# Performance work log

Measured on AMD Instinct MI355X. Metric: run time of the kernel, lower is better.

## Reference

```python
import jax, jax.numpy as jnp
import numpy as np

N_NODES = 50000
NEG_SLOPE = 0.2  # PyG GATConv default LeakyReLU slope


def gat_conv(x, src, dst, W, att_src, att_dst, bias, heads, out_ch, concat):
    """PyG-style GATConv (dropout=0, add_self_loops omitted to match raw edge list usage).
    x: [N, in], W: [in, heads*out_ch], att_*: [1, heads, out_ch], bias: [heads*out_ch] or [out_ch].
    Messages flow src -> dst; softmax normalizes over incoming edges of each dst node."""
    N = x.shape[0]
    h = (x @ W).reshape(N, heads, out_ch)                      # [N,H,C]
    a_s = (h * att_src).sum(-1)                                # [N,H]
    a_d = (h * att_dst).sum(-1)                                # [N,H]
    e = jax.nn.leaky_relu(a_s[src] + a_d[dst], NEG_SLOPE)      # [E,H] per-edge logits
    m = jax.ops.segment_max(e, dst, num_segments=N)            # [N,H] stable softmax max
    p = jnp.exp(e - m[dst])                                    # [E,H]
    s = jax.ops.segment_sum(p, dst, num_segments=N)            # [N,H]
    alpha = p / (s[dst] + 1e-16)                               # [E,H] attention coeffs
    out = jax.ops.segment_sum(h[src] * alpha[:, :, None], dst, num_segments=N)  # [N,H,C]
    out = out.reshape(N, heads * out_ch) if concat else out.mean(axis=1)
    return out + bias


def setup_inputs() -> dict:
    key = jax.random.key(0)
    ks = jax.random.split(key, 10)
    in_ch, hid, heads, out_ch = 128, 32, 4, 64
    E = 800000
    x = jax.random.normal(ks[0], (N_NODES, in_ch), dtype=jnp.float32)
    edge_index = jax.random.randint(ks[1], (2, E), 0, N_NODES, dtype=jnp.int64)
    sc = 0.1
    return {
        "x": x,
        "edge_index": edge_index,
        "W1": jax.random.normal(ks[2], (in_ch, heads * hid), dtype=jnp.float32) * sc,
        "att_src1": jax.random.normal(ks[3], (1, heads, hid), dtype=jnp.float32) * sc,
        "att_dst1": jax.random.normal(ks[4], (1, heads, hid), dtype=jnp.float32) * sc,
        "b1": jnp.zeros((heads * hid,), dtype=jnp.float32),
        "W2": jax.random.normal(ks[5], (heads * hid, out_ch), dtype=jnp.float32) * sc,
        "att_src2": jax.random.normal(ks[6], (1, 1, out_ch), dtype=jnp.float32) * sc,
        "att_dst2": jax.random.normal(ks[7], (1, 1, out_ch), dtype=jnp.float32) * sc,
        "b2": jnp.zeros((out_ch,), dtype=jnp.float32),
    }


def reference(x, edge_index, W1, att_src1, att_dst1, b1, W2, att_src2, att_dst2, b2):
    src, dst = edge_index[0], edge_index[1]
    h = gat_conv(x, src, dst, W1, att_src1, att_dst1, b1, heads=4, out_ch=32, concat=True)
    h = jax.nn.elu(h)
    out = gat_conv(h, src, dst, W2, att_src2, att_dst2, b2, heads=1, out_ch=64, concat=False)
    return out
```

## Files before the change

kernel.cpp:

```cpp
#include <hip/hip_runtime.h>

#define N_NODES 50000
#define N_EDGES 800000
#define GEMM_BLKS ((N_NODES + 63) / 64)
#define FILL_BLKS 4096
#define RANGE 6250
#define EDGES_PER_BLK 1564
#define MAXDEG 64
#define AGG_BLKS (N_NODES / 4)

typedef __attribute__((ext_vector_type(8))) short bf16x8;
typedef __attribute__((ext_vector_type(4))) float f32x4;
typedef unsigned short u16;
typedef unsigned int u32;

__device__ __forceinline__ float lrelu(float x) { return x > 0.f ? x : 0.2f * x; }

__device__ __forceinline__ u16 f2bf(float f) {
    u32 u = __float_as_uint(f);
    return (u16)((u + 0x7FFFu + ((u >> 16) & 1u)) >> 16);
}
__device__ __forceinline__ float bflo(u32 w) { return __uint_as_float(w << 16); }
__device__ __forceinline__ float bfhi(u32 w) { return __uint_as_float(w & 0xFFFF0000u); }
__device__ __forceinline__ float elu(float x) { return x > 0.f ? x : __expf(x) - 1.f; }

__global__ __launch_bounds__(256) void k_prep(
    const float* __restrict__ W1, const float* __restrict__ as1v, const float* __restrict__ ad1v,
    const float* __restrict__ W2, const float* __restrict__ as2v, const float* __restrict__ ad2v,
    u16* __restrict__ Wt1, u16* __restrict__ Wt2, int* __restrict__ deg)
{
    int gid = blockIdx.x * 256 + threadIdx.x;
    for (int i = gid; i < N_NODES; i += 112 * 256) deg[i] = 0;
    if (gid < 144 * 128) {
        int n = gid >> 7, k = gid & 127;
        float v = 0.f;
        if (n < 128) v = W1[k * 128 + n];
        else if (n < 136) {
            int h = n - 128;
            const float* att = (h < 4) ? as1v : ad1v;
            int hh = h & 3;
            float s = 0.f;
            for (int c = 0; c < 32; ++c) s += W1[k * 128 + hh * 32 + c] * att[hh * 32 + c];
            v = s;
        }
        Wt1[n * 128 + k] = f2bf(v);
    } else {
        int g2 = gid - 144 * 128;
        if (g2 < 80 * 128) {
            int n = g2 >> 7, k = g2 & 127;
            float v = 0.f;
            if (n < 64) v = W2[k * 64 + n];
            else if (n == 64) { float s = 0.f; for (int c = 0; c < 64; ++c) s += W2[k * 64 + c] * as2v[c]; v = s; }
            else if (n == 65) { float s = 0.f; for (int c = 0; c < 64; ++c) s += W2[k * 64 + c] * ad2v[c]; v = s; }
            Wt2[n * 128 + k] = f2bf(v);
        }
    }
}

__global__ __launch_bounds__(256) void k_fill(
    const int* __restrict__ src, const int* __restrict__ dst,
    int* __restrict__ deg, u16* __restrict__ col16)
{
    const int g = blockIdx.x & 7;
    const int b = blockIdx.x >> 3;
    const int lo = g * RANGE;
    const int hi = min(lo + RANGE, N_NODES);
    const int e0 = b * EDGES_PER_BLK;
    const int e1 = min(e0 + EDGES_PER_BLK, N_EDGES);
    for (int e = e0 + threadIdx.x; e < e1; e += 256) {
        int v = dst[e];
        if (v >= lo && v < hi) {
            int pos = atomicAdd(&deg[v], 1);
            if (pos < MAXDEG) col16[v * MAXDEG + pos] = (u16)src[e];
        }
    }
}

__global__ __launch_bounds__(256) void k_gemm1(
    const float* __restrict__ x, const u16* __restrict__ Wt1,
    u16* __restrict__ hbf, float* __restrict__ as_, float* __restrict__ ad_)
{
    __shared__ u16 xs[64][136];
    __shared__ u16 ws[144][136];
    const int t = threadIdx.x;
    const int n0 = blockIdx.x * 64;
    #pragma unroll
    for (int it = 0; it < 8; ++it) {
        int idx = it * 256 + t;
        int row = idx >> 5, c4 = (idx & 31) * 4;
        int n = n0 + row;
        float4 xv = make_float4(0.f, 0.f, 0.f, 0.f);
        if (n < N_NODES) xv = *(const float4*)&x[(size_t)n * 128 + c4];
        uint2 pk;
        pk.x = (u32)f2bf(xv.x) | ((u32)f2bf(xv.y) << 16);
        pk.y = (u32)f2bf(xv.z) | ((u32)f2bf(xv.w) << 16);
        *(uint2*)&xs[row][c4] = pk;
    }
    #pragma unroll
    for (int it = 0; it < 9; ++it) {
        int idx = it * 256 + t;
        int row = idx >> 4, c8 = (idx & 15) * 8;
        *(uint4*)&ws[row][c8] = *(const uint4*)&Wt1[row * 128 + c8];
    }
    __syncthreads();
    const int l = t & 63, w = t >> 6;
    const int lm = l & 15, quad = l >> 4;
    f32x4 acc[9];
    #pragma unroll
    for (int nt = 0; nt < 9; ++nt) acc[nt] = (f32x4){0.f, 0.f, 0.f, 0.f};
    const u16* arow = &xs[w * 16 + lm][0];
    #pragma unroll
    for (int kc = 0; kc < 4; ++kc) {
        int k0 = kc * 32 + quad * 8;
        bf16x8 a = *(const bf16x8*)&arow[k0];
        #pragma unroll
        for (int nt = 0; nt < 9; ++nt) {
            bf16x8 b = *(const bf16x8*)&ws[nt * 16 + lm][k0];
            acc[nt] = __builtin_amdgcn_mfma_f32_16x16x32_bf16(a, b, acc[nt], 0, 0, 0);
        }
    }
    #pragma unroll
    for (int r = 0; r < 4; ++r) {
        int n = n0 + w * 16 + quad * 4 + r;
        if (n >= N_NODES) continue;
        #pragma unroll
        for (int nt = 0; nt < 8; ++nt)
            hbf[(size_t)n * 128 + nt * 16 + lm] = f2bf(acc[nt][r]);
        if (lm < 4)      as_[n * 4 + lm]     = acc[8][r];
        else if (lm < 8) ad_[n * 4 + lm - 4] = acc[8][r];
    }
}

__global__ __launch_bounds__(256) void k_agg1(
    const int* __restrict__ deg, const u16* __restrict__ col16,
    const float* __restrict__ as_, const float* __restrict__ ad_,
    const u32* __restrict__ h1u, const float* __restrict__ b1,
    u32* __restrict__ out1u)
{
    const int t = threadIdx.x;
    const int wv = t >> 6;
    const int l = t & 63;
    const int v = blockIdx.x * 4 + wv;
    const int c = l & 15;
    const int slot = l >> 4;
    const int hh = c >> 2;
    const int dg = min(deg[v], MAXDEG);
    const float adh = ad_[v * 4 + hh];
    const u16* cr = col16 + v * MAXDEG;
    float a[8] = {0.f, 0.f, 0.f, 0.f, 0.f, 0.f, 0.f, 0.f};
    float s = 0.f;
    for (int i0 = slot; i0 < dg; i0 += 8) {
        int i1 = i0 + 4;
        bool m1 = i1 < dg;
        int u0 = cr[i0];
        int u1 = cr[m1 ? i1 : i0];
        float p0 = __expf(lrelu(as_[u0 * 4 + hh] + adh));
        float p1 = m1 ? __expf(lrelu(as_[u1 * 4 + hh] + adh)) : 0.f;
        uint4 w0 = *(const uint4*)(h1u + (u0 << 6) + (c << 2));
        uint4 w1 = *(const uint4*)(h1u + (u1 << 6) + (c << 2));
        a[0] = fmaf(p0, bflo(w0.x), a[0]); a[1] = fmaf(p0, bfhi(w0.x), a[1]);
        a[2] = fmaf(p0, bflo(w0.y), a[2]); a[3] = fmaf(p0, bfhi(w0.y), a[3]);
        a[4] = fmaf(p0, bflo(w0.z), a[4]); a[5] = fmaf(p0, bfhi(w0.z), a[5]);
        a[6] = fmaf(p0, bflo(w0.w), a[6]); a[7] = fmaf(p0, bfhi(w0.w), a[7]);
        a[0] = fmaf(p1, bflo(w1.x), a[0]); a[1] = fmaf(p1, bfhi(w1.x), a[1]);
        a[2] = fmaf(p1, bflo(w1.y), a[2]); a[3] = fmaf(p1, bfhi(w1.y), a[3]);
        a[4] = fmaf(p1, bflo(w1.z), a[4]); a[5] = fmaf(p1, bfhi(w1.z), a[5]);
        a[6] = fmaf(p1, bflo(w1.w), a[6]); a[7] = fmaf(p1, bfhi(w1.w), a[7]);
        s += p0 + p1;
    }
    #pragma unroll
    for (int k = 0; k < 8; ++k) {
        a[k] += __shfl_xor(a[k], 16);
        a[k] += __shfl_xor(a[k], 32);
    }
    s += __shfl_xor(s, 16);
    s += __shfl_xor(s, 32);
    if (slot == 0) {
        float inv = 1.f / (s + 1e-16f);
        float4 b0 = *(const float4*)&b1[8 * c];
        float4 b4 = *(const float4*)&b1[8 * c + 4];
        float o0 = elu(a[0] * inv + b0.x);
        float o1 = elu(a[1] * inv + b0.y);
        float o2 = elu(a[2] * inv + b0.z);
        float o3 = elu(a[3] * inv + b0.w);
        float o4 = elu(a[4] * inv + b4.x);
        float o5 = elu(a[5] * inv + b4.y);
        float o6 = elu(a[6] * inv + b4.z);
        float o7 = elu(a[7] * inv + b4.w);
        uint4 pk;
        pk.x = (u32)f2bf(o0) | ((u32)f2bf(o1) << 16);
        pk.y = (u32)f2bf(o2) | ((u32)f2bf(o3) << 16);
        pk.z = (u32)f2bf(o4) | ((u32)f2bf(o5) << 16);
        pk.w = (u32)f2bf(o6) | ((u32)f2bf(o7) << 16);
        *(uint4*)(out1u + v * 64 + 4 * c) = pk;
    }
}

__global__ __launch_bounds__(256) void k_gemm2(
    const u16* __restrict__ xbf, const u16* __restrict__ Wt2,
    u16* __restrict__ hbf, float* __restrict__ as_, float* __restrict__ ad_)
{
    __shared__ u16 xs[64][136];
    __shared__ u16 ws[80][136];
    const int t = threadIdx.x;
    const int n0 = blockIdx.x * 64;
    #pragma unroll
    for (int it = 0; it < 4; ++it) {
        int idx = it * 256 + t;
        int row = idx >> 4, c8 = (idx & 15) * 8;
        int n = n0 + row;
        uint4 vv = make_uint4(0u, 0u, 0u, 0u);
        if (n < N_NODES) vv = *(const uint4*)&xbf[(size_t)n * 128 + c8];
        *(uint4*)&xs[row][c8] = vv;
    }
    #pragma unroll
    for (int it = 0; it < 5; ++it) {
        int idx = it * 256 + t;
        int row = idx >> 4, c8 = (idx & 15) * 8;
        *(uint4*)&ws[row][c8] = *(const uint4*)&Wt2[row * 128 + c8];
    }
    __syncthreads();
    const int l = t & 63, w = t >> 6;
    const int lm = l & 15, quad = l >> 4;
    f32x4 acc[5];
    #pragma unroll
    for (int nt = 0; nt < 5; ++nt) acc[nt] = (f32x4){0.f, 0.f, 0.f, 0.f};
    const u16* arow = &xs[w * 16 + lm][0];
    #pragma unroll
    for (int kc = 0; kc < 4; ++kc) {
        int k0 = kc * 32 + quad * 8;
        bf16x8 a = *(const bf16x8*)&arow[k0];
        #pragma unroll
        for (int nt = 0; nt < 5; ++nt) {
            bf16x8 b = *(const bf16x8*)&ws[nt * 16 + lm][k0];
            acc[nt] = __builtin_amdgcn_mfma_f32_16x16x32_bf16(a, b, acc[nt], 0, 0, 0);
        }
    }
    #pragma unroll
    for (int r = 0; r < 4; ++r) {
        int n = n0 + w * 16 + quad * 4 + r;
        if (n >= N_NODES) continue;
        #pragma unroll
        for (int nt = 0; nt < 4; ++nt)
            hbf[(size_t)n * 64 + nt * 16 + lm] = f2bf(acc[nt][r]);
        if (lm == 0)      as_[n] = acc[4][r];
        else if (lm == 1) ad_[n] = acc[4][r];
    }
}

__global__ __launch_bounds__(256) void k_agg2(
    const int* __restrict__ deg, const u16* __restrict__ col16,
    const float* __restrict__ as_, const float* __restrict__ ad_,
    const u32* __restrict__ h2u, const float* __restrict__ b2,
    float* __restrict__ out)
{
    const int t = threadIdx.x;
    const int wv = t >> 6;
    const int l = t & 63;
    const int v = blockIdx.x * 4 + wv;
    const int c = l & 7;
    const int slot = l >> 3;
    const int dg = min(deg[v], MAXDEG);
    const float adh = ad_[v];
    const u16* cr = col16 + v * MAXDEG;
    float a[8] = {0.f, 0.f, 0.f, 0.f, 0.f, 0.f, 0.f, 0.f};
    float s = 0.f;
    for (int i0 = slot; i0 < dg; i0 += 16) {
        int i1 = i0 + 8;
        bool m1 = i1 < dg;
        int u0 = cr[i0];
        int u1 = cr[m1 ? i1 : i0];
        float p0 = __expf(lrelu(as_[u0] + adh));
        float p1 = m1 ? __expf(lrelu(as_[u1] + adh)) : 0.f;
        uint4 w0 = *(const uint4*)(h2u + (u0 << 5) + (c << 2));
        uint4 w1 = *(const uint4*)(h2u + (u1 << 5) + (c << 2));
        a[0] = fmaf(p0, bflo(w0.x), a[0]); a[1] = fmaf(p0, bfhi(w0.x), a[1]);
        a[2] = fmaf(p0, bflo(w0.y), a[2]); a[3] = fmaf(p0, bfhi(w0.y), a[3]);
        a[4] = fmaf(p0, bflo(w0.z), a[4]); a[5] = fmaf(p0, bfhi(w0.z), a[5]);
        a[6] = fmaf(p0, bflo(w0.w), a[6]); a[7] = fmaf(p0, bfhi(w0.w), a[7]);
        a[0] = fmaf(p1, bflo(w1.x), a[0]); a[1] = fmaf(p1, bfhi(w1.x), a[1]);
        a[2] = fmaf(p1, bflo(w1.y), a[2]); a[3] = fmaf(p1, bfhi(w1.y), a[3]);
        a[4] = fmaf(p1, bflo(w1.z), a[4]); a[5] = fmaf(p1, bfhi(w1.z), a[5]);
        a[6] = fmaf(p1, bflo(w1.w), a[6]); a[7] = fmaf(p1, bfhi(w1.w), a[7]);
        s += p0 + p1;
    }
    #pragma unroll
    for (int k = 0; k < 8; ++k) {
        a[k] += __shfl_xor(a[k], 8);
        a[k] += __shfl_xor(a[k], 16);
        a[k] += __shfl_xor(a[k], 32);
    }
    s += __shfl_xor(s, 8);
    s += __shfl_xor(s, 16);
    s += __shfl_xor(s, 32);
    if (slot == 0) {
        float inv = 1.f / (s + 1e-16f);
        float4 b0 = *(const float4*)&b2[8 * c];
        float4 b4 = *(const float4*)&b2[8 * c + 4];
        float4 oa, ob;
        oa.x = a[0] * inv + b0.x;
        oa.y = a[1] * inv + b0.y;
        oa.z = a[2] * inv + b0.z;
        oa.w = a[3] * inv + b0.w;
        ob.x = a[4] * inv + b4.x;
        ob.y = a[5] * inv + b4.y;
        ob.z = a[6] * inv + b4.z;
        ob.w = a[7] * inv + b4.w;
        *(float4*)&out[(size_t)v * 64 + 8 * c]     = oa;
        *(float4*)&out[(size_t)v * 64 + 8 * c + 4] = ob;
    }
}

extern "C" void kernel_launch(void* const* d_in, const int* in_sizes, int n_in,
                              void* d_out, int out_size, void* d_ws, size_t ws_size,
                              hipStream_t stream)
{
    const float* x      = (const float*)d_in[0];
    const int*   ei     = (const int*)d_in[1];
    const float* W1     = (const float*)d_in[2];
    const float* att_s1 = (const float*)d_in[3];
    const float* att_d1 = (const float*)d_in[4];
    const float* b1     = (const float*)d_in[5];
    const float* W2     = (const float*)d_in[6];
    const float* att_s2 = (const float*)d_in[7];
    const float* att_d2 = (const float*)d_in[8];
    const float* b2     = (const float*)d_in[9];
    const int* src = ei;
    const int* dst = ei + N_EDGES;
    float* out = (float*)d_out;

    char* wsp = (char*)d_ws;
    u16* Wt1   = (u16*)wsp;  wsp += 144 * 128 * 2;
    u16* Wt2   = (u16*)wsp;  wsp += 80 * 128 * 2;
    u16* h1bf  = (u16*)wsp;  wsp += (size_t)N_NODES * 128 * 2;
    u16* o1bf  = (u16*)wsp;  wsp += (size_t)N_NODES * 128 * 2;
    u16* h2bf  = (u16*)wsp;  wsp += (size_t)N_NODES * 64 * 2;
    float* as1 = (float*)wsp; wsp += (size_t)N_NODES * 4 * 4;
    float* ad1 = (float*)wsp; wsp += (size_t)N_NODES * 4 * 4;
    float* as2 = (float*)wsp; wsp += (size_t)N_NODES * 4;
    float* ad2 = (float*)wsp; wsp += (size_t)N_NODES * 4;
    int* deg   = (int*)wsp;   wsp += (size_t)N_NODES * 4;
    u16* col16 = (u16*)wsp;  wsp += (size_t)N_NODES * MAXDEG * 2;

    k_prep<<<112, 256, 0, stream>>>(W1, att_s1, att_d1, W2, att_s2, att_d2, Wt1, Wt2, deg);
    k_fill<<<FILL_BLKS, 256, 0, stream>>>(src, dst, deg, col16);

    k_gemm1<<<GEMM_BLKS, 256, 0, stream>>>(x, Wt1, h1bf, as1, ad1);
    k_agg1<<<AGG_BLKS, 256, 0, stream>>>(deg, col16, as1, ad1, (const u32*)h1bf, b1, (u32*)o1bf);

    k_gemm2<<<GEMM_BLKS, 256, 0, stream>>>(o1bf, Wt2, h2bf, as2, ad2);
    k_agg2<<<AGG_BLKS, 256, 0, stream>>>(deg, col16, as2, ad2, (const u32*)h2bf, b2, out);
}
```

Measured before the change: 204.7 us.

## Fuse fill and gemm1, read weights from global, batch aggregation gathers

```diff
diff --git a/kernel.cpp b/kernel.cpp
--- a/kernel.cpp
+++ b/kernel.cpp
@@ -8,6 +8,7 @@
 #define EDGES_PER_BLK 1564
 #define MAXDEG 64
 #define AGG_BLKS (N_NODES / 4)
+#define FG1_BLKS (GEMM_BLKS + FILL_BLKS)
 
 typedef __attribute__((ext_vector_type(8))) short bf16x8;
 typedef __attribute__((ext_vector_type(4))) float f32x4;
@@ -23,6 +24,13 @@
 __device__ __forceinline__ float bflo(u32 w) { return __uint_as_float(w << 16); }
 __device__ __forceinline__ float bfhi(u32 w) { return __uint_as_float(w & 0xFFFF0000u); }
 __device__ __forceinline__ float elu(float x) { return x > 0.f ? x : __expf(x) - 1.f; }
+
+#define FMA8(p_, w_) do { \
+    a[0] = fmaf(p_, bflo(w_.x), a[0]); a[1] = fmaf(p_, bfhi(w_.x), a[1]); \
+    a[2] = fmaf(p_, bflo(w_.y), a[2]); a[3] = fmaf(p_, bfhi(w_.y), a[3]); \
+    a[4] = fmaf(p_, bflo(w_.z), a[4]); a[5] = fmaf(p_, bfhi(w_.z), a[5]); \
+    a[6] = fmaf(p_, bflo(w_.w), a[6]); a[7] = fmaf(p_, bfhi(w_.w), a[7]); \
+} while (0)
 
 __global__ __launch_bounds__(256) void k_prep(
     const float* __restrict__ W1, const float* __restrict__ as1v, const float* __restrict__ ad1v,
@@ -57,32 +65,31 @@
     }
 }
 
-__global__ __launch_bounds__(256) void k_fill(
+__global__ __launch_bounds__(256) void k_fg1(
+    const float* __restrict__ x, const u16* __restrict__ Wt1,
+    u16* __restrict__ hbf, float* __restrict__ as_, float* __restrict__ ad_,
     const int* __restrict__ src, const int* __restrict__ dst,
     int* __restrict__ deg, u16* __restrict__ col16)
 {
-    const int g = blockIdx.x & 7;
-    const int b = blockIdx.x >> 3;
-    const int lo = g * RANGE;
-    const int hi = min(lo + RANGE, N_NODES);
-    const int e0 = b * EDGES_PER_BLK;
-    const int e1 = min(e0 + EDGES_PER_BLK, N_EDGES);
-    for (int e = e0 + threadIdx.x; e < e1; e += 256) {
-        int v = dst[e];
-        if (v >= lo && v < hi) {
-            int pos = atomicAdd(&deg[v], 1);
-            if (pos < MAXDEG) col16[v * MAXDEG + pos] = (u16)src[e];
-        }
-    }
-}
-
-__global__ __launch_bounds__(256) void k_gemm1(
-    const float* __restrict__ x, const u16* __restrict__ Wt1,
-    u16* __restrict__ hbf, float* __restrict__ as_, float* __restrict__ ad_)
-{
+    const int t = threadIdx.x;
+    if (blockIdx.x >= GEMM_BLKS) {
+        const int bb = blockIdx.x - GEMM_BLKS;
+        const int g = bb & 7;
+        const int b = bb >> 3;
+        const int lo = g * RANGE;
+        const int hi = min(lo + RANGE, N_NODES);
+        const int e0 = b * EDGES_PER_BLK;
+        const int e1 = min(e0 + EDGES_PER_BLK, N_EDGES);
+        for (int e = e0 + t; e < e1; e += 256) {
+            int v = dst[e];
+            if (v >= lo && v < hi) {
+                int pos = atomicAdd(&deg[v], 1);
+                if (pos < MAXDEG) col16[v * MAXDEG + pos] = (u16)src[e];
+            }
+        }
+        return;
+    }
     __shared__ u16 xs[64][136];
-    __shared__ u16 ws[144][136];
-    const int t = threadIdx.x;
     const int n0 = blockIdx.x * 64;
     #pragma unroll
     for (int it = 0; it < 8; ++it) {
@@ -96,12 +103,6 @@
         pk.y = (u32)f2bf(xv.z) | ((u32)f2bf(xv.w) << 16);
         *(uint2*)&xs[row][c4] = pk;
     }
-    #pragma unroll
-    for (int it = 0; it < 9; ++it) {
-        int idx = it * 256 + t;
-        int row = idx >> 4, c8 = (idx & 15) * 8;
-        *(uint4*)&ws[row][c8] = *(const uint4*)&Wt1[row * 128 + c8];
-    }
     __syncthreads();
     const int l = t & 63, w = t >> 6;
     const int lm = l & 15, quad = l >> 4;
@@ -109,13 +110,14 @@
     #pragma unroll
     for (int nt = 0; nt < 9; ++nt) acc[nt] = (f32x4){0.f, 0.f, 0.f, 0.f};
     const u16* arow = &xs[w * 16 + lm][0];
+    const u16* brow = &Wt1[lm * 128];
     #pragma unroll
     for (int kc = 0; kc < 4; ++kc) {
         int k0 = kc * 32 + quad * 8;
         bf16x8 a = *(const bf16x8*)&arow[k0];
         #pragma unroll
         for (int nt = 0; nt < 9; ++nt) {
-            bf16x8 b = *(const bf16x8*)&ws[nt * 16 + lm][k0];
+            bf16x8 b = *(const bf16x8*)&brow[nt * 2048 + k0];
             acc[nt] = __builtin_amdgcn_mfma_f32_16x16x32_bf16(a, b, acc[nt], 0, 0, 0);
         }
     }
@@ -147,26 +149,30 @@
     const int dg = min(deg[v], MAXDEG);
     const float adh = ad_[v * 4 + hh];
     const u16* cr = col16 + v * MAXDEG;
+    int colreg = (l < dg) ? (int)cr[l] : 0;
     float a[8] = {0.f, 0.f, 0.f, 0.f, 0.f, 0.f, 0.f, 0.f};
     float s = 0.f;
-    for (int i0 = slot; i0 < dg; i0 += 8) {
-        int i1 = i0 + 4;
-        bool m1 = i1 < dg;
-        int u0 = cr[i0];
-        int u1 = cr[m1 ? i1 : i0];
-        float p0 = __expf(lrelu(as_[u0 * 4 + hh] + adh));
-        float p1 = m1 ? __expf(lrelu(as_[u1 * 4 + hh] + adh)) : 0.f;
+    for (int base = 0; base < dg; base += 16) {
+        int i0 = base + slot;
+        int u0 = __shfl(colreg, i0);
+        int u1 = __shfl(colreg, i0 + 4);
+        int u2 = __shfl(colreg, i0 + 8);
+        int u3 = __shfl(colreg, i0 + 12);
+        bool m0 = i0 < dg, m1 = i0 + 4 < dg, m2 = i0 + 8 < dg, m3 = i0 + 12 < dg;
+        float e0 = as_[u0 * 4 + hh];
+        float e1 = as_[u1 * 4 + hh];
+        float e2 = as_[u2 * 4 + hh];
+        float e3 = as_[u3 * 4 + hh];
         uint4 w0 = *(const uint4*)(h1u + (u0 << 6) + (c << 2));
         uint4 w1 = *(const uint4*)(h1u + (u1 << 6) + (c << 2));
-        a[0] = fmaf(p0, bflo(w0.x), a[0]); a[1] = fmaf(p0, bfhi(w0.x), a[1]);
-        a[2] = fmaf(p0, bflo(w0.y), a[2]); a[3] = fmaf(p0, bfhi(w0.y), a[3]);
-        a[4] = fmaf(p0, bflo(w0.z), a[4]); a[5] = fmaf(p0, bfhi(w0.z), a[5]);
-        a[6] = fmaf(p0, bflo(w0.w), a[6]); a[7] = fmaf(p0, bfhi(w0.w), a[7]);
-        a[0] = fmaf(p1, bflo(w1.x), a[0]); a[1] = fmaf(p1, bfhi(w1.x), a[1]);
-        a[2] = fmaf(p1, bflo(w1.y), a[2]); a[3] = fmaf(p1, bfhi(w1.y), a[3]);
-        a[4] = fmaf(p1, bflo(w1.z), a[4]); a[5] = fmaf(p1, bfhi(w1.z), a[5]);
-        a[6] = fmaf(p1, bflo(w1.w), a[6]); a[7] = fmaf(p1, bfhi(w1.w), a[7]);
-        s += p0 + p1;
+        uint4 w2 = *(const uint4*)(h1u + (u2 << 6) + (c << 2));
+        uint4 w3 = *(const uint4*)(h1u + (u3 << 6) + (c << 2));
+        float p0 = m0 ? __expf(lrelu(e0 + adh)) : 0.f;
+        float p1 = m1 ? __expf(lrelu(e1 + adh)) : 0.f;
+        float p2 = m2 ? __expf(lrelu(e2 + adh)) : 0.f;
+        float p3 = m3 ? __expf(lrelu(e3 + adh)) : 0.f;
+        FMA8(p0, w0); FMA8(p1, w1); FMA8(p2, w2); FMA8(p3, w3);
+        s += (p0 + p1) + (p2 + p3);
     }
     #pragma unroll
     for (int k = 0; k < 8; ++k) {
@@ -201,7 +207,6 @@
     u16* __restrict__ hbf, float* __restrict__ as_, float* __restrict__ ad_)
 {
     __shared__ u16 xs[64][136];
-    __shared__ u16 ws[80][136];
     const int t = threadIdx.x;
     const int n0 = blockIdx.x * 64;
     #pragma unroll
@@ -213,12 +218,6 @@
         if (n < N_NODES) vv = *(const uint4*)&xbf[(size_t)n * 128 + c8];
         *(uint4*)&xs[row][c8] = vv;
     }
-    #pragma unroll
-    for (int it = 0; it < 5; ++it) {
-        int idx = it * 256 + t;
-        int row = idx >> 4, c8 = (idx & 15) * 8;
-        *(uint4*)&ws[row][c8] = *(const uint4*)&Wt2[row * 128 + c8];
-    }
     __syncthreads();
     const int l = t & 63, w = t >> 6;
     const int lm = l & 15, quad = l >> 4;
@@ -226,13 +225,14 @@
     #pragma unroll
     for (int nt = 0; nt < 5; ++nt) acc[nt] = (f32x4){0.f, 0.f, 0.f, 0.f};
     const u16* arow = &xs[w * 16 + lm][0];
+    const u16* brow = &Wt2[lm * 128];
     #pragma unroll
     for (int kc = 0; kc < 4; ++kc) {
         int k0 = kc * 32 + quad * 8;
         bf16x8 a = *(const bf16x8*)&arow[k0];
         #pragma unroll
         for (int nt = 0; nt < 5; ++nt) {
-            bf16x8 b = *(const bf16x8*)&ws[nt * 16 + lm][k0];
+            bf16x8 b = *(const bf16x8*)&brow[nt * 2048 + k0];
             acc[nt] = __builtin_amdgcn_mfma_f32_16x16x32_bf16(a, b, acc[nt], 0, 0, 0);
         }
     }
@@ -263,26 +263,30 @@
     const int dg = min(deg[v], MAXDEG);
     const float adh = ad_[v];
     const u16* cr = col16 + v * MAXDEG;
+    int colreg = (l < dg) ? (int)cr[l] : 0;
     float a[8] = {0.f, 0.f, 0.f, 0.f, 0.f, 0.f, 0.f, 0.f};
     float s = 0.f;
-    for (int i0 = slot; i0 < dg; i0 += 16) {
-        int i1 = i0 + 8;
-        bool m1 = i1 < dg;
-        int u0 = cr[i0];
-        int u1 = cr[m1 ? i1 : i0];
-        float p0 = __expf(lrelu(as_[u0] + adh));
-        float p1 = m1 ? __expf(lrelu(as_[u1] + adh)) : 0.f;
+    for (int base = 0; base < dg; base += 32) {
+        int i0 = base + slot;
+        int u0 = __shfl(colreg, i0);
+        int u1 = __shfl(colreg, i0 + 8);
+        int u2 = __shfl(colreg, i0 + 16);
+        int u3 = __shfl(colreg, i0 + 24);
+        bool m0 = i0 < dg, m1 = i0 + 8 < dg, m2 = i0 + 16 < dg, m3 = i0 + 24 < dg;
+        float e0 = as_[u0];
+        float e1 = as_[u1];
+        float e2 = as_[u2];
+        float e3 = as_[u3];
         uint4 w0 = *(const uint4*)(h2u + (u0 << 5) + (c << 2));
         uint4 w1 = *(const uint4*)(h2u + (u1 << 5) + (c << 2));
-        a[0] = fmaf(p0, bflo(w0.x), a[0]); a[1] = fmaf(p0, bfhi(w0.x), a[1]);
-        a[2] = fmaf(p0, bflo(w0.y), a[2]); a[3] = fmaf(p0, bfhi(w0.y), a[3]);
-        a[4] = fmaf(p0, bflo(w0.z), a[4]); a[5] = fmaf(p0, bfhi(w0.z), a[5]);
-        a[6] = fmaf(p0, bflo(w0.w), a[6]); a[7] = fmaf(p0, bfhi(w0.w), a[7]);
-        a[0] = fmaf(p1, bflo(w1.x), a[0]); a[1] = fmaf(p1, bfhi(w1.x), a[1]);
-        a[2] = fmaf(p1, bflo(w1.y), a[2]); a[3] = fmaf(p1, bfhi(w1.y), a[3]);
-        a[4] = fmaf(p1, bflo(w1.z), a[4]); a[5] = fmaf(p1, bfhi(w1.z), a[5]);
-        a[6] = fmaf(p1, bflo(w1.w), a[6]); a[7] = fmaf(p1, bfhi(w1.w), a[7]);
-        s += p0 + p1;
+        uint4 w2 = *(const uint4*)(h2u + (u2 << 5) + (c << 2));
+        uint4 w3 = *(const uint4*)(h2u + (u3 << 5) + (c << 2));
+        float p0 = m0 ? __expf(lrelu(e0 + adh)) : 0.f;
+        float p1 = m1 ? __expf(lrelu(e1 + adh)) : 0.f;
+        float p2 = m2 ? __expf(lrelu(e2 + adh)) : 0.f;
+        float p3 = m3 ? __expf(lrelu(e3 + adh)) : 0.f;
+        FMA8(p0, w0); FMA8(p1, w1); FMA8(p2, w2); FMA8(p3, w3);
+        s += (p0 + p1) + (p2 + p3);
     }
     #pragma unroll
     for (int k = 0; k < 8; ++k) {
@@ -343,9 +347,9 @@
     u16* col16 = (u16*)wsp;  wsp += (size_t)N_NODES * MAXDEG * 2;
 
     k_prep<<<112, 256, 0, stream>>>(W1, att_s1, att_d1, W2, att_s2, att_d2, Wt1, Wt2, deg);
-    k_fill<<<FILL_BLKS, 256, 0, stream>>>(src, dst, deg, col16);
-
-    k_gemm1<<<GEMM_BLKS, 256, 0, stream>>>(x, Wt1, h1bf, as1, ad1);
+
+    k_fg1<<<FG1_BLKS, 256, 0, stream>>>(x, Wt1, h1bf, as1, ad1, src, dst, deg, col16);
+
     k_agg1<<<AGG_BLKS, 256, 0, stream>>>(deg, col16, as1, ad1, (const u32*)h1bf, b1, (u32*)o1bf);
 
     k_gemm2<<<GEMM_BLKS, 256, 0, stream>>>(o1bf, Wt2, h2bf, as2, ad2);
```

New measurement: 212.4 us. 3.7% more time.
